# Kernel optimization log

Measured on AMD Instinct MI355X. Metric: run time of the kernel, lower is better.

Reference implementation:

```python
import jax, jax.numpy as jnp
import numpy as np

B, CIN, H, W = 8, 4, 64, 64
OUT = 8
K = 3            # kernel side
K2 = K * K       # ReLUKANLayer input_size
G_SIZE = 5       # grid_size
KK = 3           # spline k
G = G_SIZE + KK  # g + k = 8 phases per input element
R = 4.0 * G_SIZE * G_SIZE / ((KK + 1) * (KK + 1))  # 6.25


def setup_inputs() -> dict:
    key = jax.random.key(0)
    k1, k2, k3 = jax.random.split(key, 3)
    x = jax.random.normal(k1, (B, CIN, H, W), dtype=jnp.float32)
    # ReLUKAN phase params: one independent KAN kernel per (out_ch, in_ch)
    pl_base = (jnp.arange(-KK, G_SIZE, dtype=jnp.float32) / G_SIZE)  # (G,)
    phase_low = jnp.broadcast_to(pl_base, (OUT, CIN, K2, G)).astype(jnp.float32)
    phase_high = phase_low + (KK + 1) / G_SIZE
    # equal_size_conv of each ReLUKANLayer: full contraction over (K2, G) -> scalar, plus bias
    weight = jax.random.normal(k2, (OUT, CIN, K2, G), dtype=jnp.float32) / np.sqrt(K2 * G)
    bias = jax.random.normal(k3, (OUT, CIN), dtype=jnp.float32) * 0.01
    return {"x": x, "phase_low": phase_low, "phase_high": phase_high,
            "weight": weight, "bias": bias}


def _patches(x):
    # im2col (torch.nn.Unfold), stride 1, no padding, no dilation
    Bt, C, Ht, Wt = x.shape
    Ho, Wo = Ht - K + 1, Wt - K + 1
    p = jnp.stack([x[:, :, i:i + Ho, j:j + Wo]
                   for i in range(K) for j in range(K)], axis=-1)  # (B,C,Ho,Wo,K2)
    return p.reshape(Bt, C, Ho * Wo, K2), Ho, Wo


def reference(x, phase_low, phase_high, weight, bias):
    # patches: (B, Cin, P, K2)
    patches, Ho, Wo = _patches(x)
    xe = patches[:, None, :, :, :, None]          # (B,1,Cin,P,K2,1)
    pl = phase_low[None, :, :, None, :, :]        # (1,O,Cin,1,K2,G)
    ph = phase_high[None, :, :, None, :, :]
    # ReLUKAN spline basis: (relu(x-pl)*relu(ph-x)*r)^2
    s = (jax.nn.relu(xe - pl) * jax.nn.relu(ph - xe) * R) ** 2  # (B,O,Cin,P,K2,G)
    # full contraction per kernel (equal_size_conv with kernel (G, K2) -> scalar),
    # then accumulate over in-channels per out-channel
    out = jnp.einsum('bocpfg,ocfg->bop', s, weight) + bias.sum(axis=1)[None, :, None]
    return out.reshape(x.shape[0], weight.shape[0], Ho, Wo)
```

## Files before the change

### kernel.cpp

```cpp
#include <hip/hip_runtime.h>

#define B_   8
#define CIN_ 4
#define H_   64
#define W_   64
#define OUT_ 8
#define K_   3
#define K2_  9
#define G_   8
#define HO_  62
#define WO_  62
#define P_   (HO_ * WO_)
#define NPIX (B_ * P_)
#define NBLK ((NPIX + 63) / 64)

__global__ __launch_bounds__(512) void kan_fused(
    const float* __restrict__ x,
    const float* __restrict__ w,
    const float* __restrict__ bias,
    float* __restrict__ out)
{
    const int lane  = threadIdx.x;
    const int ohalf = threadIdx.y;
    const int c     = threadIdx.z;
    const int ob    = ohalf * 4;
    const int tid   = blockIdx.x * 64 + lane;

    const float RS[G_] = {-2.5f, 0.0f, 2.5f, 5.0f, 7.5f, 10.0f, 12.5f, 15.0f};
    const float RP[G_] = {-0.75f, -1.0f, -0.75f, 0.0f, 1.25f, 3.0f, 5.25f, 8.0f};

    float acc[4] = {0.f, 0.f, 0.f, 0.f};

    if (tid < NPIX) {
        const int b  = tid / P_;
        const int p  = tid - b * P_;
        const int oy = p / WO_;
        const int ox = p - oy * WO_;

        const float* xc = x + (size_t)(b * CIN_ + c) * (H_ * W_);
        const float* wc = w + (size_t)(ob * CIN_ + c) * (K2_ * G_);

        #pragma unroll
        for (int f = 0; f < K2_; ++f) {
            const int ki = f / 3, kj = f % 3;
            const float xv = xc[(oy + ki) * W_ + ox + kj];
            const float q  = -(6.25f * xv) * xv;
            float mm[G_];
            #pragma unroll
            for (int g = 0; g < G_; ++g) {
                const float t = fmaf(xv, RS[g], q) - RP[g];
                const float m = fmaxf(t, 0.f);
                mm[g] = m * m;
            }
            #pragma unroll
            for (int oo = 0; oo < 4; ++oo) {
                const float* wrow = wc + (size_t)(oo * CIN_) * (K2_ * G_) + f * G_;
                #pragma unroll
                for (int g = 0; g < G_; ++g)
                    acc[oo] = fmaf(mm[g], wrow[g], acc[oo]);
            }
        }
    }

    __shared__ float lds[CIN_][2][4][64];
    #pragma unroll
    for (int oo = 0; oo < 4; ++oo) lds[c][ohalf][oo][lane] = acc[oo];
    __syncthreads();

    const int t    = (threadIdx.z * 2 + threadIdx.y) * 64 + threadIdx.x;
    const int o    = t >> 6;
    const int pix  = t & 63;
    const int tid2 = blockIdx.x * 64 + pix;
    if (tid2 < NPIX) {
        float s = 0.f;
        #pragma unroll
        for (int cc = 0; cc < CIN_; ++cc) s += bias[o * CIN_ + cc];
        #pragma unroll
        for (int cc = 0; cc < CIN_; ++cc) s += lds[cc][o >> 2][o & 3][pix];
        const int b = tid2 / P_;
        const int p = tid2 - b * P_;
        out[(size_t)(b * OUT_ + o) * P_ + p] = s;
    }
}

extern "C" void kernel_launch(void* const* d_in, const int* in_sizes, int n_in,
                              void* d_out, int out_size, void* d_ws, size_t ws_size,
                              hipStream_t stream) {
    const float* x    = (const float*)d_in[0];
    const float* w    = (const float*)d_in[3];
    const float* bias = (const float*)d_in[4];
    float* out = (float*)d_out;

    kan_fused<<<dim3(NBLK), dim3(64, 2, 4), 0, stream>>>(x, w, bias, out);
}
```

Before: 70.57 us.

## Split work across phase halves instead of output halves to cut redundant basis math

Each thread now computes four of the eight spline phases for all eight output channels, where it previously computed all eight phases for four outputs. The basis values are no longer computed twice per pixel, and the y/z indices go through readfirstlane so weight addresses are wave-uniform scalar loads. The cost is twice as many accumulators and LDS partials, plus a reduction over both phase halves and all channels. Phase constants are now derived in-kernel from the wave-uniform half index.

```diff
diff --git a/kernel.cpp b/kernel.cpp
--- a/kernel.cpp
+++ b/kernel.cpp
@@ -20,16 +20,20 @@
     const float* __restrict__ bias,
     float* __restrict__ out)
 {
-    const int lane  = threadIdx.x;
-    const int ohalf = threadIdx.y;
-    const int c     = threadIdx.z;
-    const int ob    = ohalf * 4;
-    const int tid   = blockIdx.x * 64 + lane;
+    const int lane = threadIdx.x;
+    const int gh = __builtin_amdgcn_readfirstlane(threadIdx.y);
+    const int c  = __builtin_amdgcn_readfirstlane(threadIdx.z);
+    const int tid = blockIdx.x * 64 + lane;
 
-    const float RS[G_] = {-2.5f, 0.0f, 2.5f, 5.0f, 7.5f, 10.0f, 12.5f, 15.0f};
-    const float RP[G_] = {-0.75f, -1.0f, -0.75f, 0.0f, 1.25f, 3.0f, 5.25f, 8.0f};
+    float RSg[4], RPg[4];
+    #pragma unroll
+    for (int j = 0; j < 4; ++j) {
+        const float g = (float)(gh * 4 + j);
+        RSg[j] = fmaf(2.5f, g, -2.5f);
+        RPg[j] = 0.25f * (g - 3.0f) * (g + 1.0f);
+    }
 
-    float acc[4] = {0.f, 0.f, 0.f, 0.f};
+    float acc[OUT_] = {0.f, 0.f, 0.f, 0.f, 0.f, 0.f, 0.f, 0.f};
 
     if (tid < NPIX) {
         const int b  = tid / P_;
@@ -37,49 +41,50 @@
         const int oy = p / WO_;
         const int ox = p - oy * WO_;
 
-        const float* xc = x + (size_t)(b * CIN_ + c) * (H_ * W_);
-        const float* wc = w + (size_t)(ob * CIN_ + c) * (K2_ * G_);
+        const float* xr = x + (size_t)(b * CIN_ + c) * (H_ * W_) + oy * W_ + ox;
+        const float* wc = w + c * (K2_ * G_) + gh * 4;
 
         #pragma unroll
         for (int f = 0; f < K2_; ++f) {
             const int ki = f / 3, kj = f % 3;
-            const float xv = xc[(oy + ki) * W_ + ox + kj];
+            const float xv = xr[ki * W_ + kj];
             const float q  = -(6.25f * xv) * xv;
-            float mm[G_];
+            float mm[4];
             #pragma unroll
-            for (int g = 0; g < G_; ++g) {
-                const float t = fmaf(xv, RS[g], q) - RP[g];
+            for (int j = 0; j < 4; ++j) {
+                const float t = fmaf(xv, RSg[j], q) - RPg[j];
                 const float m = fmaxf(t, 0.f);
-                mm[g] = m * m;
+                mm[j] = m * m;
             }
             #pragma unroll
-            for (int oo = 0; oo < 4; ++oo) {
-                const float* wrow = wc + (size_t)(oo * CIN_) * (K2_ * G_) + f * G_;
+            for (int oo = 0; oo < OUT_; ++oo) {
+                const float* wrow = wc + oo * (CIN_ * K2_ * G_) + f * G_;
                 #pragma unroll
-                for (int g = 0; g < G_; ++g)
-                    acc[oo] = fmaf(mm[g], wrow[g], acc[oo]);
+                for (int j = 0; j < 4; ++j)
+                    acc[oo] = fmaf(mm[j], wrow[j], acc[oo]);
             }
         }
     }
 
-    __shared__ float lds[CIN_][2][4][64];
+    __shared__ float lds[CIN_][2][OUT_][64];
     #pragma unroll
-    for (int oo = 0; oo < 4; ++oo) lds[c][ohalf][oo][lane] = acc[oo];
+    for (int oo = 0; oo < OUT_; ++oo) lds[c][gh][oo][lane] = acc[oo];
     __syncthreads();
 
-    const int t    = (threadIdx.z * 2 + threadIdx.y) * 64 + threadIdx.x;
-    const int o    = t >> 6;
-    const int pix  = t & 63;
+    const int o    = c * 2 + gh;
+    const int pix  = lane;
     const int tid2 = blockIdx.x * 64 + pix;
     if (tid2 < NPIX) {
-        float s = 0.f;
+        float s = bias[o * CIN_ + 0] + bias[o * CIN_ + 1]
+                + bias[o * CIN_ + 2] + bias[o * CIN_ + 3];
         #pragma unroll
-        for (int cc = 0; cc < CIN_; ++cc) s += bias[o * CIN_ + cc];
-        #pragma unroll
-        for (int cc = 0; cc < CIN_; ++cc) s += lds[cc][o >> 2][o & 3][pix];
-        const int b = tid2 / P_;
-        const int p = tid2 - b * P_;
-        out[(size_t)(b * OUT_ + o) * P_ + p] = s;
+        for (int cc = 0; cc < CIN_; ++cc)
+            #pragma unroll
+            for (int g2 = 0; g2 < 2; ++g2)
+                s += lds[cc][g2][o][pix];
+        const int b2 = tid2 / P_;
+        const int p2 = tid2 - b2 * P_;
+        out[(size_t)(b2 * OUT_ + o) * P_ + p2] = s;
     }
 }
 
```

Result: faster. 67.19 us (-4.8%).
